# Kernel optimization log

Measured on AMD Instinct MI355X. Metric: run time of the kernel, lower is better.

The kernel has to match this reference:

```python
import jax, jax.numpy as jnp
import numpy as np

N_NODES = 8192
IN_F = 256
OUT_F = 256
ALPHA = 0.2  # LeakyReLU negative slope


def setup_inputs() -> dict:
    key = jax.random.key(0)
    k1, k2, k3, k4 = jax.random.split(key, 4)
    X = jax.random.normal(k1, (N_NODES, IN_F), dtype=jnp.float32)
    A = jax.random.randint(k2, (N_NODES, N_NODES), 0, 2, dtype=jnp.int32)
    # torch nn.Linear weight layout: (out_features, in_features)
    W = jax.random.normal(k3, (OUT_F, IN_F), dtype=jnp.float32) * (1.0 / np.sqrt(IN_F))
    r = jax.random.normal(k4, (2 * OUT_F, 1), dtype=jnp.float32)
    return {"X": X, "A": A, "W": W, "r": r}


def reference(X, A, W, r):
    # Wh = X @ W^T  -> (N, F_out)
    Wh = X @ W.T
    # Split r so that cat([Wh_i, Wh_j]) @ r == Wh_i @ r_src + Wh_j @ r_dst
    F_out = Wh.shape[-1]
    r_src = r[:F_out, 0]   # (F,)
    r_dst = r[F_out:, 0]   # (F,)
    s_i = Wh @ r_src       # (N,)
    s_j = Wh @ r_dst       # (N,)
    e = s_i[:, None] + s_j[None, :]                      # (N, N)
    e = jnp.where(e >= 0, e, ALPHA * e)                  # LeakyReLU
    e = jnp.where(A == 0, -jnp.inf, e)                   # mask non-edges
    attention = jax.nn.softmax(e, axis=1)                # row-wise softmax
    output = attention @ Wh                              # (N, F_out)
    return jax.nn.gelu(output, approximate=False)        # torch F.gelu (exact)
```

## Files before the change

### kernel.cpp

```cpp
#include <hip/hip_runtime.h>
#include <hip/hip_bf16.h>

#define N_NODES 8192
#define NF      256
#define L2E     1.44269504088896341f

typedef __attribute__((ext_vector_type(8))) short short8;
typedef __attribute__((ext_vector_type(4))) short short4v;
typedef __attribute__((ext_vector_type(4))) float floatx4;

static __device__ __forceinline__ float bf2f(short s) {
    return __uint_as_float(((unsigned)(unsigned short)s) << 16);
}
static __device__ __forceinline__ short f2bf_rn(float f) {
    unsigned u = __float_as_uint(f) + 0x8000u;
    return (short)(u >> 16);
}
struct bfpair { short hi, lo; };
static __device__ __forceinline__ bfpair split_bf(float x) {
    bfpair p;
    p.hi = f2bf_rn(x);
    p.lo = f2bf_rn(x - bf2f(p.hi));
    return p;
}
static __device__ __forceinline__ void async16(const void* g, void* l) {
    __builtin_amdgcn_global_load_lds(
        (const __attribute__((address_space(1))) unsigned*)g,
        (__attribute__((address_space(3))) unsigned*)l, 16, 0, 0);
}

__global__ __launch_bounds__(256) void kx_split(const float* __restrict__ W,
                                                short* __restrict__ Whi,
                                                short* __restrict__ Wlo) {
    #pragma unroll
    for (int e = 0; e < 4; ++e) {
        const int i = blockIdx.x * 1024 + e * 256 + threadIdx.x;
        bfpair p = split_bf(W[i]);
        Whi[i] = p.hi;
        Wlo[i] = p.lo;
    }
}

__global__ __launch_bounds__(512) void k1_gemm(const float* __restrict__ X,
                                               const short* __restrict__ Whi,
                                               const short* __restrict__ Wlo,
                                               const float* __restrict__ r,
                                               short* __restrict__ WhT,
                                               float* __restrict__ sp_src,
                                               float* __restrict__ sp_dst) {
    __shared__ float Xs[32 * 256];

    const int tid = threadIdx.x;
    const int w = tid >> 6, lane = tid & 63;
    const int q = lane >> 4, m = lane & 15;
    const int rh = w >> 2, cq = w & 3;
    const int i_base = blockIdx.x * 32;

    #pragma unroll
    for (int v = 0; v < 4; ++v) {
        const int rowv = w * 4 + v;
        const int c = lane ^ (rowv & 7);
        async16(X + (size_t)(i_base + rowv) * NF + c * 4, &Xs[rowv * 256]);
    }
    __syncthreads();

    floatx4 acc[4] = {};
    const int xrow = rh * 16 + m;
    const int r7 = xrow & 7;
    #pragma unroll
    for (int ks = 0; ks < 8; ++ks) {
        const int c0 = ks * 8 + q * 2;
        float4 f0 = *(const float4*)(&Xs[xrow * 256 + ((c0 ^ r7) * 4)]);
        float4 f1 = *(const float4*)(&Xs[xrow * 256 + (((c0 + 1) ^ r7) * 4)]);
        const float xsv[8] = {f0.x, f0.y, f0.z, f0.w, f1.x, f1.y, f1.z, f1.w};
        short8 xh, xl;
        #pragma unroll
        for (int c = 0; c < 8; ++c) {
            bfpair p = split_bf(xsv[c]);
            xh[c] = p.hi; xl[c] = p.lo;
        }
        #pragma unroll
        for (int nt = 0; nt < 4; ++nt) {
            const int n = cq * 64 + nt * 16 + m;
            short8 wh = *(const short8*)(Whi + n * NF + ks * 32 + q * 8);
            short8 wl = *(const short8*)(Wlo + n * NF + ks * 32 + q * 8);
            acc[nt] = __builtin_amdgcn_mfma_f32_16x16x32_bf16(xh, wh, acc[nt], 0, 0, 0);
            acc[nt] = __builtin_amdgcn_mfma_f32_16x16x32_bf16(xl, wh, acc[nt], 0, 0, 0);
            acc[nt] = __builtin_amdgcn_mfma_f32_16x16x32_bf16(xh, wl, acc[nt], 0, 0, 0);
        }
    }

    const int i0 = i_base + rh * 16 + q * 4;
    float vs[4] = {0.f, 0.f, 0.f, 0.f}, vd[4] = {0.f, 0.f, 0.f, 0.f};
    #pragma unroll
    for (int nt = 0; nt < 4; ++nt) {
        const int n = cq * 64 + nt * 16 + m;
        short4v v;
        #pragma unroll
        for (int r2 = 0; r2 < 4; ++r2) v[r2] = f2bf_rn(acc[nt][r2]);
        *(short4v*)(WhT + (size_t)n * N_NODES + i0) = v;
        const float rs = r[n], rd = r[NF + n];
        #pragma unroll
        for (int r2 = 0; r2 < 4; ++r2) {
            vs[r2] = fmaf(acc[nt][r2], rs, vs[r2]);
            vd[r2] = fmaf(acc[nt][r2], rd, vd[r2]);
        }
    }
    #pragma unroll
    for (int mask = 1; mask <= 8; mask <<= 1) {
        #pragma unroll
        for (int r2 = 0; r2 < 4; ++r2) {
            vs[r2] += __shfl_xor(vs[r2], mask);
            vd[r2] += __shfl_xor(vd[r2], mask);
        }
    }
    if (m == 0) {
        #pragma unroll
        for (int r2 = 0; r2 < 4; ++r2) {
            sp_src[cq * N_NODES + i0 + r2] = vs[r2];
            sp_dst[cq * N_NODES + i0 + r2] = vd[r2];
        }
    }
}

__global__ __launch_bounds__(256) void k2_sv(const float* __restrict__ sp_src,
                                             const float* __restrict__ sp_dst,
                                             float* __restrict__ s_src,
                                             float* __restrict__ s_dst,
                                             float* __restrict__ pmax) {
    __shared__ float red[256];
    const int tid = threadIdx.x;
    const int i = blockIdx.x * 256 + tid;
    float ss = 0.f, sd = 0.f;
    #pragma unroll
    for (int nb = 0; nb < 4; ++nb) {
        ss += sp_src[nb * N_NODES + i];
        sd += sp_dst[nb * N_NODES + i];
    }
    s_src[i] = ss;
    s_dst[i] = sd;
    red[tid] = sd;
    __syncthreads();
    for (int off = 128; off > 0; off >>= 1) {
        if (tid < off) red[tid] = fmaxf(red[tid], red[tid + off]);
        __syncthreads();
    }
    if (tid == 0) pmax[blockIdx.x] = red[0];
}

static __device__ __forceinline__ void pgroup(const int4 a, const floatx4 t,
                                              const float s_i, const float d_i,
                                              float* p) {
    const int av[4] = {a.x, a.y, a.z, a.w};
    #pragma unroll
    for (int c = 0; c < 4; ++c) {
        float sum = s_i + t[c];
        float lr  = fmaxf(sum, 0.2f * sum);
        float pp  = __builtin_amdgcn_exp2f(fmaf(lr, L2E, d_i));
        p[c] = (av[c] != 0) ? pp : 0.0f;
    }
}

__global__ __launch_bounds__(512, 4) void k4_attn(const int* __restrict__ Adj,
                                                  const short* __restrict__ WhT,
                                                  const float* __restrict__ s_dst,
                                                  const float* __restrict__ s_src,
                                                  const float* __restrict__ pmax,
                                                  float* __restrict__ pden,
                                                  float* __restrict__ outacc) {
    __shared__ union {
        short B[2][256][64];
        float red[8 * 8 * 4 * 64];
    } sm;
    __shared__ float denred[64];

    const int tid = threadIdx.x;
    const int w = tid >> 6, lane = tid & 63;
    const int q = lane >> 4, m = lane & 15;
    const int rh = w >> 2, ch = (w >> 1) & 1, jq = w & 1;
    const int ib = blockIdx.x & 255;
    const int jh = blockIdx.x >> 8;
    const int i0 = ib * 32;
    const int jbase = jh * 4096;
    const int row = i0 + rh * 16 + m;

    float M = pmax[0];
    #pragma unroll
    for (int b = 1; b < 32; ++b) M = fmaxf(M, pmax[b]);
    const float s_i = s_src[row];
    const float e0 = s_i + M;
    const float d_i = -fmaxf(e0, 0.2f * e0) * L2E;

    const int srow = lane >> 3;
    const int scc = (lane & 7) ^ srow;
    const short* gB[4];
    #pragma unroll
    for (int v = 0; v < 4; ++v)
        gB[v] = WhT + (size_t)(w * 32 + v * 8 + srow) * N_NODES + jbase + scc * 8;

    const int* Ap = Adj + (size_t)row * N_NODES + jbase + jq * 32 + q * 8;
    const float* tp = s_dst + jbase + jq * 32 + q * 8;

    floatx4 acc[8];
    #pragma unroll
    for (int nt = 0; nt < 8; ++nt) acc[nt] = (floatx4){0.f, 0.f, 0.f, 0.f};
    float den = 0.f;

    #pragma unroll
    for (int v = 0; v < 4; ++v)
        async16(gB[v], &sm.B[0][w * 32 + v * 8][0]);
    int4 a0 = *(const int4*)(Ap);
    int4 a1 = *(const int4*)(Ap + 4);
    floatx4 t0 = *(const floatx4*)(tp);
    floatx4 t1 = *(const floatx4*)(tp + 4);
    __syncthreads();

    for (int s = 0; s < 64; ++s) {
        const int cur = s & 1;

        short* dstb = &sm.B[cur ^ 1][0][0];
        const int go = ((s + 1) & 63) * 64;
        #pragma unroll
        for (int v = 0; v < 4; ++v)
            async16(gB[v] + go, dstb + (w * 32 + v * 8) * 64);
        __builtin_amdgcn_sched_barrier(0);

        int4 na0 = *(const int4*)(Ap + go);
        int4 na1 = *(const int4*)(Ap + go + 4);
        floatx4 nt0 = *(const floatx4*)(tp + go);
        floatx4 nt1 = *(const floatx4*)(tp + go + 4);
        __builtin_amdgcn_sched_barrier(0);

        float p[8];
        pgroup(a0, t0, s_i, d_i, p);
        pgroup(a1, t1, s_i, d_i, p + 4);

        short8 af;
        #pragma unroll
        for (int c = 0; c < 8; ++c) af[c] = f2bf_rn(p[c]);
        #pragma unroll
        for (int c = 0; c < 8; ++c) den += p[c];

        const short* Bb = &sm.B[cur][0][0];
        __builtin_amdgcn_s_setprio(1);
        #pragma unroll
        for (int nt = 0; nt < 8; ++nt) {
            const int n = ch * 128 + nt * 16 + m;
            const int sc = (jq * 4 + q) ^ (m & 7);
            short8 b0 = *(const short8*)(Bb + n * 64 + sc * 8);
            acc[nt] = __builtin_amdgcn_mfma_f32_16x16x32_bf16(af, b0, acc[nt], 0, 0, 0);
        }
        __builtin_amdgcn_s_setprio(0);

        __builtin_amdgcn_sched_barrier(0);
        asm volatile("s_waitcnt vmcnt(4)" ::: "memory");
        __builtin_amdgcn_s_barrier();

        a0 = na0; a1 = na1; t0 = nt0; t1 = nt1;
    }

    den += __shfl_xor(den, 16);
    den += __shfl_xor(den, 32);
    if (ch == 0 && lane < 16) denred[rh * 32 + jq * 16 + lane] = den;
    #pragma unroll
    for (int nt = 0; nt < 8; ++nt)
        #pragma unroll
        for (int rg = 0; rg < 4; ++rg)
            sm.red[((w * 8 + nt) * 4 + rg) * 64 + lane] = acc[nt][rg];
    __syncthreads();

    if (w == 0 && lane < 32) {
        const int rr = lane >> 4, mm = lane & 15;
        pden[jh * N_NODES + i0 + rr * 16 + mm] =
            denred[rr * 32 + mm] + denred[rr * 32 + 16 + mm];
    }
    if (jq == 0) {
        #pragma unroll
        for (int nt = 0; nt < 8; ++nt) {
            #pragma unroll
            for (int rg = 0; rg < 4; ++rg) {
                float v = sm.red[((w * 8 + nt) * 4 + rg) * 64 + lane]
                        + sm.red[(((w + 1) * 8 + nt) * 4 + rg) * 64 + lane];
                const int orow = i0 + rh * 16 + q * 4 + rg;
                const int n = ch * 128 + nt * 16 + m;
                atomicAdd(&outacc[(size_t)orow * NF + n], v);
            }
        }
    }
}

__global__ __launch_bounds__(256) void k5_fin(const float* __restrict__ pden,
                                              float* __restrict__ out) {
    const int gid = blockIdx.x * 256 + threadIdx.x;
    const int row = gid >> 5;
    const int c0 = (gid & 31) * 8;
    const float d = pden[row] + pden[N_NODES + row];
    const float inv = 1.0f / fmaxf(d, 1e-30f);
    float* p = out + (size_t)row * NF + c0;
    float4 v0 = *(const float4*)(p);
    float4 v1 = *(const float4*)(p + 4);
    float xs[8] = {v0.x, v0.y, v0.z, v0.w, v1.x, v1.y, v1.z, v1.w};
    #pragma unroll
    for (int c = 0; c < 8; ++c) {
        const float x = xs[c] * inv;
        xs[c] = 0.5f * x * (1.0f + erff(x * 0.70710678118f));
    }
    *(float4*)(p)     = (float4){xs[0], xs[1], xs[2], xs[3]};
    *(float4*)(p + 4) = (float4){xs[4], xs[5], xs[6], xs[7]};
}

extern "C" void kernel_launch(void* const* d_in, const int* in_sizes, int n_in,
                              void* d_out, int out_size, void* d_ws, size_t ws_size,
                              hipStream_t stream) {
    const float* X = (const float*)d_in[0];
    const int*   A = (const int*)d_in[1];
    const float* W = (const float*)d_in[2];
    const float* r = (const float*)d_in[3];
    float* out = (float*)d_out;

    char* wsp = (char*)d_ws;
    short* WhT    = (short*)wsp;                    wsp += (size_t)NF * N_NODES * 2;
    short* Whi    = (short*)wsp;                    wsp += NF * NF * 2;
    short* Wlo    = (short*)wsp;                    wsp += NF * NF * 2;
    float* sp_src = (float*)wsp;                    wsp += 4 * N_NODES * 4;
    float* sp_dst = (float*)wsp;                    wsp += 4 * N_NODES * 4;
    float* s_src  = (float*)wsp;                    wsp += N_NODES * 4;
    float* s_dst  = (float*)wsp;                    wsp += N_NODES * 4;
    float* pmax   = (float*)wsp;
    float* pden   = sp_src;

    hipMemsetAsync(out, 0, (size_t)N_NODES * NF * 4, stream);
    kx_split<<<64, 256, 0, stream>>>(W, Whi, Wlo);
    k1_gemm<<<256, 512, 0, stream>>>(X, Whi, Wlo, r, WhT, sp_src, sp_dst);
    k2_sv<<<32, 256, 0, stream>>>(sp_src, sp_dst, s_src, s_dst, pmax);
    k4_attn<<<512, 512, 0, stream>>>(A, WhT, s_dst, s_src, pmax, pden, out);
    k5_fin<<<1024, 256, 0, stream>>>(pden, out);
}
```

Baseline: 478.9 us.

## Load Wh tiles directly from global into registers, dropping LDS staging and barriers

The shared-memory double buffer for the WhT tile, its async copies and the per-iteration barrier are removed. Each lane now loads its MFMA B operand straight from global memory (relying on L2/L1 reuse across the 4 waves sharing columns), and the LDS is used only for the final reduction. This removes barrier synchronisation and LDS traffic but multiplies global/L2 load requests and exposes load latency, since the B loads are no longer prefetched an iteration ahead.

```diff
diff --git a/kernel.cpp b/kernel.cpp
--- a/kernel.cpp
+++ b/kernel.cpp
@@ -168,10 +168,7 @@
                                                   const float* __restrict__ pmax,
                                                   float* __restrict__ pden,
                                                   float* __restrict__ outacc) {
-    __shared__ union {
-        short B[2][256][64];
-        float red[8 * 8 * 4 * 64];
-    } sm;
+    __shared__ float red[8 * 8 * 4 * 64];
     __shared__ float denred[64];
 
     const int tid = threadIdx.x;
@@ -191,12 +188,12 @@
     const float e0 = s_i + M;
     const float d_i = -fmaxf(e0, 0.2f * e0) * L2E;
 
-    const int srow = lane >> 3;
-    const int scc = (lane & 7) ^ srow;
-    const short* gB[4];
-    #pragma unroll
-    for (int v = 0; v < 4; ++v)
-        gB[v] = WhT + (size_t)(w * 32 + v * 8 + srow) * N_NODES + jbase + scc * 8;
+    const short* gBn[8];
+    #pragma unroll
+    for (int nt = 0; nt < 8; ++nt) {
+        const int n = ch * 128 + nt * 16 + m;
+        gBn[nt] = WhT + (size_t)n * N_NODES + jbase + jq * 32 + q * 8;
+    }
 
     const int* Ap = Adj + (size_t)row * N_NODES + jbase + jq * 32 + q * 8;
     const float* tp = s_dst + jbase + jq * 32 + q * 8;
@@ -206,29 +203,25 @@
     for (int nt = 0; nt < 8; ++nt) acc[nt] = (floatx4){0.f, 0.f, 0.f, 0.f};
     float den = 0.f;
 
-    #pragma unroll
-    for (int v = 0; v < 4; ++v)
-        async16(gB[v], &sm.B[0][w * 32 + v * 8][0]);
     int4 a0 = *(const int4*)(Ap);
     int4 a1 = *(const int4*)(Ap + 4);
     floatx4 t0 = *(const floatx4*)(tp);
     floatx4 t1 = *(const floatx4*)(tp + 4);
-    __syncthreads();
 
     for (int s = 0; s < 64; ++s) {
-        const int cur = s & 1;
-
-        short* dstb = &sm.B[cur ^ 1][0][0];
-        const int go = ((s + 1) & 63) * 64;
-        #pragma unroll
-        for (int v = 0; v < 4; ++v)
-            async16(gB[v] + go, dstb + (w * 32 + v * 8) * 64);
+        const int go = s * 64;
+
+        short8 cb[8];
+        #pragma unroll
+        for (int nt = 0; nt < 8; ++nt)
+            cb[nt] = *(const short8*)(gBn[nt] + go);
         __builtin_amdgcn_sched_barrier(0);
 
-        int4 na0 = *(const int4*)(Ap + go);
-        int4 na1 = *(const int4*)(Ap + go + 4);
-        floatx4 nt0 = *(const floatx4*)(tp + go);
-        floatx4 nt1 = *(const floatx4*)(tp + go + 4);
+        const int gn = ((s + 1) & 63) * 64;
+        int4 na0 = *(const int4*)(Ap + gn);
+        int4 na1 = *(const int4*)(Ap + gn + 4);
+        floatx4 nt0 = *(const floatx4*)(tp + gn);
+        floatx4 nt1 = *(const floatx4*)(tp + gn + 4);
         __builtin_amdgcn_sched_barrier(0);
 
         float p[8];
@@ -241,20 +234,11 @@
         #pragma unroll
         for (int c = 0; c < 8; ++c) den += p[c];
 
-        const short* Bb = &sm.B[cur][0][0];
         __builtin_amdgcn_s_setprio(1);
         #pragma unroll
-        for (int nt = 0; nt < 8; ++nt) {
-            const int n = ch * 128 + nt * 16 + m;
-            const int sc = (jq * 4 + q) ^ (m & 7);
-            short8 b0 = *(const short8*)(Bb + n * 64 + sc * 8);
-            acc[nt] = __builtin_amdgcn_mfma_f32_16x16x32_bf16(af, b0, acc[nt], 0, 0, 0);
-        }
+        for (int nt = 0; nt < 8; ++nt)
+            acc[nt] = __builtin_amdgcn_mfma_f32_16x16x32_bf16(af, cb[nt], acc[nt], 0, 0, 0);
         __builtin_amdgcn_s_setprio(0);
-
-        __builtin_amdgcn_sched_barrier(0);
-        asm volatile("s_waitcnt vmcnt(4)" ::: "memory");
-        __builtin_amdgcn_s_barrier();
 
         a0 = na0; a1 = na1; t0 = nt0; t1 = nt1;
     }
@@ -266,7 +250,7 @@
     for (int nt = 0; nt < 8; ++nt)
         #pragma unroll
         for (int rg = 0; rg < 4; ++rg)
-            sm.red[((w * 8 + nt) * 4 + rg) * 64 + lane] = acc[nt][rg];
+            red[((w * 8 + nt) * 4 + rg) * 64 + lane] = acc[nt][rg];
     __syncthreads();
 
     if (w == 0 && lane < 32) {
@@ -279,8 +263,8 @@
         for (int nt = 0; nt < 8; ++nt) {
             #pragma unroll
             for (int rg = 0; rg < 4; ++rg) {
-                float v = sm.red[((w * 8 + nt) * 4 + rg) * 64 + lane]
-                        + sm.red[(((w + 1) * 8 + nt) * 4 + rg) * 64 + lane];
+                float v = red[((w * 8 + nt) * 4 + rg) * 64 + lane]
+                        + red[(((w + 1) * 8 + nt) * 4 + rg) * 64 + lane];
                 const int orow = i0 + rh * 16 + q * 4 + rg;
                 const int n = ch * 128 + nt * 16 + m;
                 atomicAdd(&outacc[(size_t)orow * NF + n], v);
```

New measurement: 629.8 us. 31.5% more time.

## Give each wave full 64-column K-steps and split columns four ways

Applied to the files above, without the earlier changes.

Each block now covers 64 rows and a 2048-column slice (four column splits instead of two). Every wave handles all 64 columns of a step with two MFMAs, where before pairs of waves split the columns and merged results. This removes the LDS cross-wave reduction and its barrier, and halves WhT tile reloads per row. In exchange, every wave issues its own atomic adds, which doubles global atomic traffic to the output accumulator. The s_dst loads are no longer prefetched a step ahead, and the finish kernel now sums four partial denominators.

```diff
diff --git a/kernel.cpp b/kernel.cpp
--- a/kernel.cpp
+++ b/kernel.cpp
@@ -168,20 +168,16 @@
                                                   const float* __restrict__ pmax,
                                                   float* __restrict__ pden,
                                                   float* __restrict__ outacc) {
-    __shared__ union {
-        short B[2][256][64];
-        float red[8 * 8 * 4 * 64];
-    } sm;
-    __shared__ float denred[64];
+    __shared__ short Bs[2][256][64];
 
     const int tid = threadIdx.x;
     const int w = tid >> 6, lane = tid & 63;
     const int q = lane >> 4, m = lane & 15;
-    const int rh = w >> 2, ch = (w >> 1) & 1, jq = w & 1;
-    const int ib = blockIdx.x & 255;
-    const int jh = blockIdx.x >> 8;
-    const int i0 = ib * 32;
-    const int jbase = jh * 4096;
+    const int rh = w >> 1, ch = w & 1;
+    const int ib = blockIdx.x & 127;
+    const int jh = blockIdx.x >> 7;
+    const int i0 = ib * 64;
+    const int jbase = jh * 2048;
     const int row = i0 + rh * 16 + m;
 
     float M = pmax[0];
@@ -198,8 +194,8 @@
     for (int v = 0; v < 4; ++v)
         gB[v] = WhT + (size_t)(w * 32 + v * 8 + srow) * N_NODES + jbase + scc * 8;
 
-    const int* Ap = Adj + (size_t)row * N_NODES + jbase + jq * 32 + q * 8;
-    const float* tp = s_dst + jbase + jq * 32 + q * 8;
+    const int* Ap = Adj + (size_t)row * N_NODES + jbase + q * 8;
+    const float* tp = s_dst + jbase + q * 8;
 
     floatx4 acc[8];
     #pragma unroll
@@ -208,47 +204,58 @@
 
     #pragma unroll
     for (int v = 0; v < 4; ++v)
-        async16(gB[v], &sm.B[0][w * 32 + v * 8][0]);
+        async16(gB[v], &Bs[0][w * 32 + v * 8][0]);
     int4 a0 = *(const int4*)(Ap);
     int4 a1 = *(const int4*)(Ap + 4);
-    floatx4 t0 = *(const floatx4*)(tp);
-    floatx4 t1 = *(const floatx4*)(tp + 4);
+    int4 a2 = *(const int4*)(Ap + 32);
+    int4 a3 = *(const int4*)(Ap + 36);
     __syncthreads();
 
-    for (int s = 0; s < 64; ++s) {
+    for (int s = 0; s < 32; ++s) {
         const int cur = s & 1;
-
-        short* dstb = &sm.B[cur ^ 1][0][0];
-        const int go = ((s + 1) & 63) * 64;
+        const int gt = s * 64;
+
+        floatx4 t0 = *(const floatx4*)(tp + gt);
+        floatx4 t1 = *(const floatx4*)(tp + gt + 4);
+        floatx4 t2 = *(const floatx4*)(tp + gt + 32);
+        floatx4 t3 = *(const floatx4*)(tp + gt + 36);
+        __builtin_amdgcn_sched_barrier(0);
+
+        short* dstb = &Bs[cur ^ 1][0][0];
+        const int gn = ((s + 1) & 31) * 64;
         #pragma unroll
         for (int v = 0; v < 4; ++v)
-            async16(gB[v] + go, dstb + (w * 32 + v * 8) * 64);
+            async16(gB[v] + gn, dstb + (w * 32 + v * 8) * 64);
         __builtin_amdgcn_sched_barrier(0);
 
-        int4 na0 = *(const int4*)(Ap + go);
-        int4 na1 = *(const int4*)(Ap + go + 4);
-        floatx4 nt0 = *(const floatx4*)(tp + go);
-        floatx4 nt1 = *(const floatx4*)(tp + go + 4);
+        int4 na0 = *(const int4*)(Ap + gn);
+        int4 na1 = *(const int4*)(Ap + gn + 4);
+        int4 na2 = *(const int4*)(Ap + gn + 32);
+        int4 na3 = *(const int4*)(Ap + gn + 36);
         __builtin_amdgcn_sched_barrier(0);
 
-        float p[8];
+        float p[16];
         pgroup(a0, t0, s_i, d_i, p);
         pgroup(a1, t1, s_i, d_i, p + 4);
-
-        short8 af;
-        #pragma unroll
-        for (int c = 0; c < 8; ++c) af[c] = f2bf_rn(p[c]);
-        #pragma unroll
-        for (int c = 0; c < 8; ++c) den += p[c];
-
-        const short* Bb = &sm.B[cur][0][0];
+        pgroup(a2, t2, s_i, d_i, p + 8);
+        pgroup(a3, t3, s_i, d_i, p + 12);
+
+        short8 af0, af1;
+        #pragma unroll
+        for (int c = 0; c < 8; ++c) { af0[c] = f2bf_rn(p[c]); af1[c] = f2bf_rn(p[8 + c]); }
+        #pragma unroll
+        for (int c = 0; c < 16; ++c) den += p[c];
+
+        const short* Bb = &Bs[cur][0][0];
         __builtin_amdgcn_s_setprio(1);
         #pragma unroll
         for (int nt = 0; nt < 8; ++nt) {
             const int n = ch * 128 + nt * 16 + m;
-            const int sc = (jq * 4 + q) ^ (m & 7);
-            short8 b0 = *(const short8*)(Bb + n * 64 + sc * 8);
-            acc[nt] = __builtin_amdgcn_mfma_f32_16x16x32_bf16(af, b0, acc[nt], 0, 0, 0);
+            const int sw = m & 7;
+            short8 b0 = *(const short8*)(Bb + n * 64 + ((q ^ sw) * 8));
+            short8 b1 = *(const short8*)(Bb + n * 64 + (((4 + q) ^ sw) * 8));
+            acc[nt] = __builtin_amdgcn_mfma_f32_16x16x32_bf16(af0, b0, acc[nt], 0, 0, 0);
+            acc[nt] = __builtin_amdgcn_mfma_f32_16x16x32_bf16(af1, b1, acc[nt], 0, 0, 0);
         }
         __builtin_amdgcn_s_setprio(0);
 
@@ -256,35 +263,20 @@
         asm volatile("s_waitcnt vmcnt(4)" ::: "memory");
         __builtin_amdgcn_s_barrier();
 
-        a0 = na0; a1 = na1; t0 = nt0; t1 = nt1;
+        a0 = na0; a1 = na1; a2 = na2; a3 = na3;
     }
 
     den += __shfl_xor(den, 16);
     den += __shfl_xor(den, 32);
-    if (ch == 0 && lane < 16) denred[rh * 32 + jq * 16 + lane] = den;
-    #pragma unroll
-    for (int nt = 0; nt < 8; ++nt)
-        #pragma unroll
-        for (int rg = 0; rg < 4; ++rg)
-            sm.red[((w * 8 + nt) * 4 + rg) * 64 + lane] = acc[nt][rg];
-    __syncthreads();
-
-    if (w == 0 && lane < 32) {
-        const int rr = lane >> 4, mm = lane & 15;
-        pden[jh * N_NODES + i0 + rr * 16 + mm] =
-            denred[rr * 32 + mm] + denred[rr * 32 + 16 + mm];
-    }
-    if (jq == 0) {
-        #pragma unroll
-        for (int nt = 0; nt < 8; ++nt) {
-            #pragma unroll
-            for (int rg = 0; rg < 4; ++rg) {
-                float v = sm.red[((w * 8 + nt) * 4 + rg) * 64 + lane]
-                        + sm.red[(((w + 1) * 8 + nt) * 4 + rg) * 64 + lane];
-                const int orow = i0 + rh * 16 + q * 4 + rg;
-                const int n = ch * 128 + nt * 16 + m;
-                atomicAdd(&outacc[(size_t)orow * NF + n], v);
-            }
+    if (ch == 0 && q == 0) pden[jh * N_NODES + row] = den;
+
+    #pragma unroll
+    for (int nt = 0; nt < 8; ++nt) {
+        #pragma unroll
+        for (int rg = 0; rg < 4; ++rg) {
+            const int orow = i0 + rh * 16 + q * 4 + rg;
+            const int n = ch * 128 + nt * 16 + m;
+            atomicAdd(&outacc[(size_t)orow * NF + n], acc[nt][rg]);
         }
     }
 }
@@ -294,7 +286,8 @@
     const int gid = blockIdx.x * 256 + threadIdx.x;
     const int row = gid >> 5;
     const int c0 = (gid & 31) * 8;
-    const float d = pden[row] + pden[N_NODES + row];
+    const float d = (pden[row] + pden[N_NODES + row]) +
+                    (pden[2 * N_NODES + row] + pden[3 * N_NODES + row]);
     const float inv = 1.0f / fmaxf(d, 1e-30f);
     float* p = out + (size_t)row * NF + c0;
     float4 v0 = *(const float4*)(p);
```

Result: no change. 476.9 us (-0.4%).
